# Performance work log

Hardware: AMD Instinct MI355X
Metric: run time of the kernel (lower is better)

Reference implementation:

```python
import jax, jax.numpy as jnp
import numpy as np

BATCH_SIZE = 4
TEMPERATURE = 0.07
NEG_MASK_VAL = -10.0


def setup_inputs() -> dict:
    key = jax.random.key(0)
    k1, k2 = jax.random.split(key)
    N, D = 16384, 256  # N = batch_size * n_patches
    feat_q = jax.random.normal(k1, (N, D), dtype=jnp.float32)
    feat_k = jax.random.normal(k2, (N, D), dtype=jnp.float32)
    return {"feat_q": feat_q, "feat_k": feat_k}


def reference(feat_q, feat_k):
    N, d = feat_q.shape
    feat_k = jax.lax.stop_gradient(feat_k)  # detach
    # positive logits: dot of matching rows -> [N, 1]
    l_pos = jnp.einsum('nd,nd->n', feat_q, feat_k)[:, None]
    q = feat_q.reshape(BATCH_SIZE, -1, d)  # [B, P, D]
    k = feat_k.reshape(BATCH_SIZE, -1, d)
    P = q.shape[1]
    # intra-batch-element negatives: [B, P, P]
    l_neg = jnp.einsum('bpd,bqd->bpq', q, k)
    eye = jnp.eye(P, dtype=bool)[None, :, :]
    l_neg = jnp.where(eye, jnp.float32(NEG_MASK_VAL), l_neg).reshape(-1, P)
    out = jnp.concatenate([l_pos, l_neg], axis=1) / TEMPERATURE  # [N, 1+P]
    # cross-entropy with target class 0, reduction='none'
    loss = -jax.nn.log_softmax(out, axis=1)[:, 0]
    return loss
```

## Files before the change

kernel.cpp:

```cpp
#include <hip/hip_runtime.h>
#include <hip/hip_bf16.h>


typedef __attribute__((ext_vector_type(8))) short short8;
typedef __attribute__((ext_vector_type(4))) float f32x4;

#define BATCH 4
#define PN 4096
#define DD 256
#define BN 64

constexpr float kLog2e = 1.4426950408889634f;
constexpr float kScale = kLog2e / 0.07f;
constexpr float kMask2 = -10.0f * kScale;
constexpr float kLn2   = 0.6931471805599453f;
constexpr float kNegInf = -3.0e38f;

__device__ __forceinline__ unsigned short f2bf(float f) {
  __hip_bfloat16 h = __float2bfloat16(f);
  return *reinterpret_cast<unsigned short*>(&h);
}
__device__ __forceinline__ float fexp2(float x) { return exp2f(x); }
__device__ __forceinline__ float flog2(float x) { return log2f(x); }

__global__ void k_convert(const float* __restrict__ src,
                          unsigned short* __restrict__ dst, int n4) {
  int i = blockIdx.x * blockDim.x + threadIdx.x;
  if (i >= n4) return;
  float4 v = reinterpret_cast<const float4*>(src)[i];
  ushort4 o;
  o.x = f2bf(v.x); o.y = f2bf(v.y); o.z = f2bf(v.z); o.w = f2bf(v.w);
  reinterpret_cast<ushort4*>(dst)[i] = o;
}

__device__ __forceinline__ void stage_tile(const char* __restrict__ src,
                                           char* ldsbase, int tid) {
  const int wv = tid >> 6;
#pragma unroll
  for (int ip = 0; ip < 8; ip++) {
    const int o   = ip * 4096 + tid * 16;
    const int row = o >> 9;
    const int so  = o ^ ((row & 15) << 4);
    __builtin_amdgcn_global_load_lds(
        (const __attribute__((address_space(1))) void*)(src + so),
        (__attribute__((address_space(3))) void*)(ldsbase + ip * 4096 + wv * 1024),
        16, 0, 0);
  }
}

__global__ __launch_bounds__(256, 2) void k_nce_split(
    const float* __restrict__ fq, const unsigned short* __restrict__ kb,
    float* __restrict__ pl, float* __restrict__ pp) {
  __shared__ __align__(16) char kt[2][BN * DD * 2];

  const int blk = blockIdx.x;
  const int b   = blk & 3;
  const int rt  = (blk >> 2) & 31;
  const int kc  = blk >> 7;
  const int R0  = rt * 128;
  const int tid = threadIdx.x;
  const int w   = tid >> 6;
  const int l   = tid & 63;
  const int g   = l >> 4;
  const int li  = l & 15;

  short8 a[2][8];
#pragma unroll
  for (int af = 0; af < 2; af++) {
    const float* qrow =
        fq + ((size_t)(b * PN + R0 + w * 32 + af * 16 + li)) * DD;
#pragma unroll
    for (int ks = 0; ks < 8; ks++) {
      const float* p = qrow + ks * 32 + g * 8;
      float4 v0 = *reinterpret_cast<const float4*>(p);
      float4 v1 = *reinterpret_cast<const float4*>(p + 4);
      a[af][ks][0] = (short)f2bf(v0.x * kScale);
      a[af][ks][1] = (short)f2bf(v0.y * kScale);
      a[af][ks][2] = (short)f2bf(v0.z * kScale);
      a[af][ks][3] = (short)f2bf(v0.w * kScale);
      a[af][ks][4] = (short)f2bf(v1.x * kScale);
      a[af][ks][5] = (short)f2bf(v1.y * kScale);
      a[af][ks][6] = (short)f2bf(v1.z * kScale);
      a[af][ks][7] = (short)f2bf(v1.w * kScale);
    }
  }

  float m[2][4], lsum[2][4], pos[2][4];
#pragma unroll
  for (int af = 0; af < 2; af++)
#pragma unroll
    for (int r = 0; r < 4; r++) {
      m[af][r] = kNegInf; lsum[af][r] = 0.f; pos[af][r] = kNegInf;
    }

  const char* ksrc = reinterpret_cast<const char*>(kb) +
                     (size_t)b * PN * 512 + (size_t)kc * 16 * 32768;
  const int diag_gt = (R0 + w * 32) >> 6;

  stage_tile(ksrc, kt[0], tid);
  __syncthreads();

  for (int ct = 0; ct < 16; ct++) {
    const int cur = ct & 1;
    if (ct + 1 < 16) stage_tile(ksrc + (size_t)(ct + 1) * 32768, kt[cur ^ 1], tid);

    const char* lb = kt[cur];
    f32x4 acc[2][4];
#pragma unroll
    for (int af = 0; af < 2; af++)
#pragma unroll
      for (int cf = 0; cf < 4; cf++) acc[af][cf] = f32x4{0.f, 0.f, 0.f, 0.f};

#pragma unroll
    for (int ks = 0; ks < 8; ks++) {
#pragma unroll
      for (int cf = 0; cf < 4; cf++) {
        const int row = cf * 16 + li;
        const int off = row * 512 + ((ks * 64 + g * 16) ^ ((row & 15) << 4));
        short8 bf = *reinterpret_cast<const short8*>(lb + off);
        acc[0][cf] =
            __builtin_amdgcn_mfma_f32_16x16x32_bf16(a[0][ks], bf, acc[0][cf], 0, 0, 0);
        acc[1][cf] =
            __builtin_amdgcn_mfma_f32_16x16x32_bf16(a[1][ks], bf, acc[1][cf], 0, 0, 0);
      }
    }

    const int gt = kc * 16 + ct;
    if (gt == diag_gt) {
#pragma unroll
      for (int af = 0; af < 2; af++) {
        const int cfd = ((w & 1) << 1) + af;
#pragma unroll
        for (int cf = 0; cf < 4; cf++)
          if (cf == cfd) {
#pragma unroll
            for (int r = 0; r < 4; r++)
              if (li == g * 4 + r) { pos[af][r] = acc[af][cf][r]; acc[af][cf][r] = kMask2; }
          }
      }
    }

#pragma unroll
    for (int af = 0; af < 2; af++)
#pragma unroll
      for (int r = 0; r < 4; r++) {
        float v0 = acc[af][0][r], v1 = acc[af][1][r];
        float v2 = acc[af][2][r], v3 = acc[af][3][r];
        float t0 = fmaxf(fmaxf(v0, v1), fmaxf(v2, v3));
        float mo = m[af][r];
        float mn = fmaxf(mo, t0);
        float s = fexp2(v0 - mn) + fexp2(v1 - mn) + fexp2(v2 - mn) + fexp2(v3 - mn);
        lsum[af][r] = lsum[af][r] * fexp2(mo - mn) + s;
        m[af][r] = mn;
      }
    __syncthreads();
  }

  const bool diag_chunk = (kc == (rt >> 3));
#pragma unroll
  for (int af = 0; af < 2; af++)
#pragma unroll
    for (int r = 0; r < 4; r++) {
      float m_ = m[af][r], l_ = lsum[af][r], p_ = pos[af][r];
#pragma unroll
      for (int off = 1; off < 16; off <<= 1) {
        float mo = __shfl_xor(m_, off, 64);
        float lo = __shfl_xor(l_, off, 64);
        float po = __shfl_xor(p_, off, 64);
        float mn = fmaxf(m_, mo);
        l_ = l_ * fexp2(m_ - mn) + lo * fexp2(mo - mn);
        m_ = mn;
        p_ = fmaxf(p_, po);
      }
      if (li == 0) {
        const int rowg = b * PN + R0 + w * 32 + af * 16 + g * 4 + r;
        pl[kc * (BATCH * PN) + rowg] = m_ + flog2(l_);
        if (diag_chunk) pp[rowg] = p_;
      }
    }
}

__global__ void k_combine(const float* __restrict__ pl,
                          const float* __restrict__ pp,
                          float* __restrict__ out) {
  const int i = blockIdx.x * blockDim.x + threadIdx.x;
  if (i >= BATCH * PN) return;
  float a0 = pl[i], a1 = pl[BATCH * PN + i];
  float a2 = pl[2 * BATCH * PN + i], a3 = pl[3 * BATCH * PN + i];
  float p = pp[i];
  float mm = fmaxf(fmaxf(a0, a1), fmaxf(a2, a3));
  float s = fexp2(a0 - mm) + fexp2(a1 - mm) + fexp2(a2 - mm) + fexp2(a3 - mm);
  float lse = mm + flog2(s);
  float mn = fmaxf(lse, p);
  float la = mn + flog2(fexp2(lse - mn) + fexp2(p - mn));
  out[i] = (la - p) * kLn2;
}

__global__ __launch_bounds__(256) void k_nce_full(const float* __restrict__ fq,
                                                  const unsigned short* __restrict__ kb,
                                                  float* __restrict__ out) {
  __shared__ __align__(16) char kt[2][BN * DD * 2];
  const int blk = blockIdx.x;
  const int b = blk & 3, rt = blk >> 2;
  const int R0 = rt * 64;
  const int tid = threadIdx.x;
  const int w = tid >> 6, l = tid & 63, g = l >> 4, li = l & 15;

  const float* qrow = fq + ((size_t)(b * PN + R0 + w * 16 + li)) * DD;
  short8 a[8];
#pragma unroll
  for (int ks = 0; ks < 8; ks++) {
    const float* p = qrow + ks * 32 + g * 8;
    float4 v0 = *reinterpret_cast<const float4*>(p);
    float4 v1 = *reinterpret_cast<const float4*>(p + 4);
    a[ks][0] = (short)f2bf(v0.x * kScale); a[ks][1] = (short)f2bf(v0.y * kScale);
    a[ks][2] = (short)f2bf(v0.z * kScale); a[ks][3] = (short)f2bf(v0.w * kScale);
    a[ks][4] = (short)f2bf(v1.x * kScale); a[ks][5] = (short)f2bf(v1.y * kScale);
    a[ks][6] = (short)f2bf(v1.z * kScale); a[ks][7] = (short)f2bf(v1.w * kScale);
  }
  float m[4], lsum[4], pos[4];
#pragma unroll
  for (int r = 0; r < 4; r++) { m[r] = kNegInf; lsum[r] = 0.f; pos[r] = kNegInf; }
  const char* ksrc = reinterpret_cast<const char*>(kb + (size_t)b * PN * DD);
  stage_tile(ksrc, kt[0], tid);
  __syncthreads();
  for (int ct = 0; ct < 64; ct++) {
    const int cur = ct & 1;
    if (ct + 1 < 64) stage_tile(ksrc + (size_t)(ct + 1) * 32768, kt[cur ^ 1], tid);
    const char* lb = kt[cur];
    f32x4 acc[4];
#pragma unroll
    for (int cf = 0; cf < 4; cf++) acc[cf] = f32x4{0.f, 0.f, 0.f, 0.f};
#pragma unroll
    for (int ks = 0; ks < 8; ks++) {
#pragma unroll
      for (int cf = 0; cf < 4; cf++) {
        const int row = cf * 16 + li;
        const int off = row * 512 + ((ks * 64 + g * 16) ^ ((row & 15) << 4));
        short8 bf = *reinterpret_cast<const short8*>(lb + off);
        acc[cf] = __builtin_amdgcn_mfma_f32_16x16x32_bf16(a[ks], bf, acc[cf], 0, 0, 0);
      }
    }
    if (ct == rt) {
#pragma unroll
      for (int cf = 0; cf < 4; cf++)
        if (cf == w) {
#pragma unroll
          for (int r = 0; r < 4; r++)
            if (li == g * 4 + r) { pos[r] = acc[cf][r]; acc[cf][r] = kMask2; }
        }
    }
#pragma unroll
    for (int r = 0; r < 4; r++) {
      float t0 = fmaxf(fmaxf(acc[0][r], acc[1][r]), fmaxf(acc[2][r], acc[3][r]));
      float mo = m[r];
      float mn = fmaxf(mo, t0);
      float s = fexp2(acc[0][r] - mn) + fexp2(acc[1][r] - mn) +
                fexp2(acc[2][r] - mn) + fexp2(acc[3][r] - mn);
      lsum[r] = lsum[r] * fexp2(mo - mn) + s;
      m[r] = mn;
    }
    __syncthreads();
  }
#pragma unroll
  for (int r = 0; r < 4; r++) {
    float m_ = m[r], l_ = lsum[r], p_ = pos[r];
#pragma unroll
    for (int off = 1; off < 16; off <<= 1) {
      float mo = __shfl_xor(m_, off, 64);
      float lo = __shfl_xor(l_, off, 64);
      float po = __shfl_xor(p_, off, 64);
      float mn = fmaxf(m_, mo);
      l_ = l_ * fexp2(m_ - mn) + lo * fexp2(mo - mn);
      m_ = mn;
      p_ = fmaxf(p_, po);
    }
    float mn  = fmaxf(m_, p_);
    float lse = mn + flog2(l_ * fexp2(m_ - mn) + fexp2(p_ - mn));
    if (li == 0) out[b * PN + R0 + w * 16 + g * 4 + r] = (lse - p_) * kLn2;
  }
}

extern "C" void kernel_launch(void* const* d_in, const int* in_sizes, int n_in,
                              void* d_out, int out_size, void* d_ws, size_t ws_size,
                              hipStream_t stream) {
  const float* fq = (const float*)d_in[0];
  const float* fk = (const float*)d_in[1];
  float* out = (float*)d_out;
  unsigned short* kb = (unsigned short*)d_ws;
  const size_t kbBytes = (size_t)BATCH * PN * DD * 2;
  const size_t plBytes = (size_t)4 * BATCH * PN * 4;
  const size_t ppBytes = (size_t)BATCH * PN * 4;

  const int n4 = (BATCH * PN * DD) / 4;
  hipLaunchKernelGGL(k_convert, dim3(n4 / 256), dim3(256), 0, stream, fk, kb, n4);

  if (ws_size >= kbBytes + plBytes + ppBytes) {
    float* pl = (float*)((char*)d_ws + kbBytes);
    float* pp = (float*)((char*)d_ws + kbBytes + plBytes);
    hipLaunchKernelGGL(k_nce_split, dim3(512), dim3(256), 0, stream, fq, kb, pl, pp);
    hipLaunchKernelGGL(k_combine, dim3((BATCH * PN) / 256), dim3(256), 0, stream,
                       pl, pp, out);
  } else {
    hipLaunchKernelGGL(k_nce_full, dim3(BATCH * (PN / 64)), dim3(256), 0, stream,
                       fq, kb, out);
  }
}
```

Before: 67.67 us.

## Enlarge row tile to 256 with 8-way column split to improve LDS reuse

Adds a new kernel in which each block processes 256 query rows (64 per wave, four A fragments) against a 512-column chunk of keys, giving an 8-way column split. Each B fragment read from LDS now feeds four MFMAs instead of two, which halves LDS traffic per FLOP and halves total key-tile staging. The first key tile load is also issued before the query conversion so the two overlap. In exchange, register pressure rises (4x8 A fragments plus 16 accumulators) and the combine kernel must merge 8 partial log-sum-exps instead of 4.

```diff
diff --git a/kernel.cpp b/kernel.cpp
--- a/kernel.cpp
+++ b/kernel.cpp
@@ -9,6 +9,7 @@
 #define PN 4096
 #define DD 256
 #define BN 64
+#define NP (BATCH * PN)
 
 constexpr float kLog2e = 1.4426950408889634f;
 constexpr float kScale = kLog2e / 0.07f;
@@ -48,27 +49,34 @@
   }
 }
 
-__global__ __launch_bounds__(256, 2) void k_nce_split(
+__global__ __launch_bounds__(256, 2) void k_nce4(
     const float* __restrict__ fq, const unsigned short* __restrict__ kb,
     float* __restrict__ pl, float* __restrict__ pp) {
   __shared__ __align__(16) char kt[2][BN * DD * 2];
 
   const int blk = blockIdx.x;
   const int b   = blk & 3;
-  const int rt  = (blk >> 2) & 31;
-  const int kc  = blk >> 7;
-  const int R0  = rt * 128;
+  const int r2  = blk >> 2;
+  const int rt  = r2 & 15;
+  const int kc  = r2 >> 4;
+  const int R0  = rt * 256;
+  const int C0  = kc * 512;
   const int tid = threadIdx.x;
   const int w   = tid >> 6;
   const int l   = tid & 63;
   const int g   = l >> 4;
   const int li  = l & 15;
 
-  short8 a[2][8];
-#pragma unroll
-  for (int af = 0; af < 2; af++) {
+  const char* ksrc = reinterpret_cast<const char*>(kb) +
+                     ((size_t)b * PN + C0) * 512;
+
+  stage_tile(ksrc, kt[0], tid);
+
+  short8 a[4][8];
+#pragma unroll
+  for (int af = 0; af < 4; af++) {
     const float* qrow =
-        fq + ((size_t)(b * PN + R0 + w * 32 + af * 16 + li)) * DD;
+        fq + ((size_t)(b * PN + R0 + w * 64 + af * 16 + li)) * DD;
 #pragma unroll
     for (int ks = 0; ks < 8; ks++) {
       const float* p = qrow + ks * 32 + g * 8;
@@ -85,29 +93,26 @@
     }
   }
 
-  float m[2][4], lsum[2][4], pos[2][4];
-#pragma unroll
-  for (int af = 0; af < 2; af++)
+  float m[4][4], lsum[4][4], pos[4][4];
+#pragma unroll
+  for (int af = 0; af < 4; af++)
 #pragma unroll
     for (int r = 0; r < 4; r++) {
       m[af][r] = kNegInf; lsum[af][r] = 0.f; pos[af][r] = kNegInf;
     }
 
-  const char* ksrc = reinterpret_cast<const char*>(kb) +
-                     (size_t)b * PN * 512 + (size_t)kc * 16 * 32768;
-  const int diag_gt = (R0 + w * 32) >> 6;
-
-  stage_tile(ksrc, kt[0], tid);
+  const int ctd = (kc == (rt >> 1)) ? ((rt & 1) * 4 + w) : -1;
+
   __syncthreads();
 
-  for (int ct = 0; ct < 16; ct++) {
+  for (int ct = 0; ct < 8; ct++) {
     const int cur = ct & 1;
-    if (ct + 1 < 16) stage_tile(ksrc + (size_t)(ct + 1) * 32768, kt[cur ^ 1], tid);
+    if (ct + 1 < 8) stage_tile(ksrc + (size_t)(ct + 1) * 32768, kt[cur ^ 1], tid);
 
     const char* lb = kt[cur];
-    f32x4 acc[2][4];
-#pragma unroll
-    for (int af = 0; af < 2; af++)
+    f32x4 acc[4][4];
+#pragma unroll
+    for (int af = 0; af < 4; af++)
 #pragma unroll
       for (int cf = 0; cf < 4; cf++) acc[af][cf] = f32x4{0.f, 0.f, 0.f, 0.f};
 
@@ -118,30 +123,23 @@
         const int row = cf * 16 + li;
         const int off = row * 512 + ((ks * 64 + g * 16) ^ ((row & 15) << 4));
         short8 bf = *reinterpret_cast<const short8*>(lb + off);
-        acc[0][cf] =
-            __builtin_amdgcn_mfma_f32_16x16x32_bf16(a[0][ks], bf, acc[0][cf], 0, 0, 0);
-        acc[1][cf] =
-            __builtin_amdgcn_mfma_f32_16x16x32_bf16(a[1][ks], bf, acc[1][cf], 0, 0, 0);
-      }
-    }
-
-    const int gt = kc * 16 + ct;
-    if (gt == diag_gt) {
-#pragma unroll
-      for (int af = 0; af < 2; af++) {
-        const int cfd = ((w & 1) << 1) + af;
-#pragma unroll
-        for (int cf = 0; cf < 4; cf++)
-          if (cf == cfd) {
-#pragma unroll
-            for (int r = 0; r < 4; r++)
-              if (li == g * 4 + r) { pos[af][r] = acc[af][cf][r]; acc[af][cf][r] = kMask2; }
-          }
-      }
-    }
-
-#pragma unroll
-    for (int af = 0; af < 2; af++)
+#pragma unroll
+        for (int af = 0; af < 4; af++)
+          acc[af][cf] = __builtin_amdgcn_mfma_f32_16x16x32_bf16(a[af][ks], bf,
+                                                               acc[af][cf], 0, 0, 0);
+      }
+    }
+
+    if (ct == ctd) {
+#pragma unroll
+      for (int af = 0; af < 4; af++)
+#pragma unroll
+        for (int r = 0; r < 4; r++)
+          if (li == g * 4 + r) { pos[af][r] = acc[af][af][r]; acc[af][af][r] = kMask2; }
+    }
+
+#pragma unroll
+    for (int af = 0; af < 4; af++)
 #pragma unroll
       for (int r = 0; r < 4; r++) {
         float v0 = acc[af][0][r], v1 = acc[af][1][r];
@@ -156,9 +154,9 @@
     __syncthreads();
   }
 
-  const bool diag_chunk = (kc == (rt >> 3));
-#pragma unroll
-  for (int af = 0; af < 2; af++)
+  const bool diag_chunk = (kc == (rt >> 1));
+#pragma unroll
+  for (int af = 0; af < 4; af++)
 #pragma unroll
     for (int r = 0; r < 4; r++) {
       float m_ = m[af][r], l_ = lsum[af][r], p_ = pos[af][r];
@@ -173,27 +171,145 @@
         p_ = fmaxf(p_, po);
       }
       if (li == 0) {
-        const int rowg = b * PN + R0 + w * 32 + af * 16 + g * 4 + r;
-        pl[kc * (BATCH * PN) + rowg] = m_ + flog2(l_);
+        const int rowg = b * PN + R0 + w * 64 + af * 16 + g * 4 + r;
+        pl[kc * NP + rowg] = m_ + flog2(l_);
         if (diag_chunk) pp[rowg] = p_;
       }
     }
 }
 
+template <int NC>
 __global__ void k_combine(const float* __restrict__ pl,
                           const float* __restrict__ pp,
                           float* __restrict__ out) {
   const int i = blockIdx.x * blockDim.x + threadIdx.x;
-  if (i >= BATCH * PN) return;
-  float a0 = pl[i], a1 = pl[BATCH * PN + i];
-  float a2 = pl[2 * BATCH * PN + i], a3 = pl[3 * BATCH * PN + i];
+  if (i >= NP) return;
+  float mm = kNegInf;
+  float v[NC];
+#pragma unroll
+  for (int c = 0; c < NC; c++) { v[c] = pl[c * NP + i]; mm = fmaxf(mm, v[c]); }
+  float s = 0.f;
+#pragma unroll
+  for (int c = 0; c < NC; c++) s += fexp2(v[c] - mm);
+  float lse = mm + flog2(s);
   float p = pp[i];
-  float mm = fmaxf(fmaxf(a0, a1), fmaxf(a2, a3));
-  float s = fexp2(a0 - mm) + fexp2(a1 - mm) + fexp2(a2 - mm) + fexp2(a3 - mm);
-  float lse = mm + flog2(s);
   float mn = fmaxf(lse, p);
   float la = mn + flog2(fexp2(lse - mn) + fexp2(p - mn));
   out[i] = (la - p) * kLn2;
+}
+
+__global__ __launch_bounds__(256, 2) void k_nce_split(
+    const float* __restrict__ fq, const unsigned short* __restrict__ kb,
+    float* __restrict__ pl, float* __restrict__ pp) {
+  __shared__ __align__(16) char kt[2][BN * DD * 2];
+  const int blk = blockIdx.x;
+  const int b   = blk & 3;
+  const int rt  = (blk >> 2) & 31;
+  const int kc  = blk >> 7;
+  const int R0  = rt * 128;
+  const int tid = threadIdx.x;
+  const int w   = tid >> 6;
+  const int l   = tid & 63;
+  const int g   = l >> 4;
+  const int li  = l & 15;
+
+  short8 a[2][8];
+#pragma unroll
+  for (int af = 0; af < 2; af++) {
+    const float* qrow = fq + ((size_t)(b * PN + R0 + w * 32 + af * 16 + li)) * DD;
+#pragma unroll
+    for (int ks = 0; ks < 8; ks++) {
+      const float* p = qrow + ks * 32 + g * 8;
+      float4 v0 = *reinterpret_cast<const float4*>(p);
+      float4 v1 = *reinterpret_cast<const float4*>(p + 4);
+      a[af][ks][0] = (short)f2bf(v0.x * kScale); a[af][ks][1] = (short)f2bf(v0.y * kScale);
+      a[af][ks][2] = (short)f2bf(v0.z * kScale); a[af][ks][3] = (short)f2bf(v0.w * kScale);
+      a[af][ks][4] = (short)f2bf(v1.x * kScale); a[af][ks][5] = (short)f2bf(v1.y * kScale);
+      a[af][ks][6] = (short)f2bf(v1.z * kScale); a[af][ks][7] = (short)f2bf(v1.w * kScale);
+    }
+  }
+  float m[2][4], lsum[2][4], pos[2][4];
+#pragma unroll
+  for (int af = 0; af < 2; af++)
+#pragma unroll
+    for (int r = 0; r < 4; r++) { m[af][r] = kNegInf; lsum[af][r] = 0.f; pos[af][r] = kNegInf; }
+
+  const char* ksrc = reinterpret_cast<const char*>(kb) +
+                     (size_t)b * PN * 512 + (size_t)kc * 16 * 32768;
+  const int diag_gt = (R0 + w * 32) >> 6;
+  stage_tile(ksrc, kt[0], tid);
+  __syncthreads();
+  for (int ct = 0; ct < 16; ct++) {
+    const int cur = ct & 1;
+    if (ct + 1 < 16) stage_tile(ksrc + (size_t)(ct + 1) * 32768, kt[cur ^ 1], tid);
+    const char* lb = kt[cur];
+    f32x4 acc[2][4];
+#pragma unroll
+    for (int af = 0; af < 2; af++)
+#pragma unroll
+      for (int cf = 0; cf < 4; cf++) acc[af][cf] = f32x4{0.f, 0.f, 0.f, 0.f};
+#pragma unroll
+    for (int ks = 0; ks < 8; ks++) {
+#pragma unroll
+      for (int cf = 0; cf < 4; cf++) {
+        const int row = cf * 16 + li;
+        const int off = row * 512 + ((ks * 64 + g * 16) ^ ((row & 15) << 4));
+        short8 bf = *reinterpret_cast<const short8*>(lb + off);
+        acc[0][cf] = __builtin_amdgcn_mfma_f32_16x16x32_bf16(a[0][ks], bf, acc[0][cf], 0, 0, 0);
+        acc[1][cf] = __builtin_amdgcn_mfma_f32_16x16x32_bf16(a[1][ks], bf, acc[1][cf], 0, 0, 0);
+      }
+    }
+    const int gt = kc * 16 + ct;
+    if (gt == diag_gt) {
+#pragma unroll
+      for (int af = 0; af < 2; af++) {
+        const int cfd = ((w & 1) << 1) + af;
+#pragma unroll
+        for (int cf = 0; cf < 4; cf++)
+          if (cf == cfd) {
+#pragma unroll
+            for (int r = 0; r < 4; r++)
+              if (li == g * 4 + r) { pos[af][r] = acc[af][cf][r]; acc[af][cf][r] = kMask2; }
+          }
+      }
+    }
+#pragma unroll
+    for (int af = 0; af < 2; af++)
+#pragma unroll
+      for (int r = 0; r < 4; r++) {
+        float v0 = acc[af][0][r], v1 = acc[af][1][r];
+        float v2 = acc[af][2][r], v3 = acc[af][3][r];
+        float t0 = fmaxf(fmaxf(v0, v1), fmaxf(v2, v3));
+        float mo = m[af][r];
+        float mn = fmaxf(mo, t0);
+        float s = fexp2(v0 - mn) + fexp2(v1 - mn) + fexp2(v2 - mn) + fexp2(v3 - mn);
+        lsum[af][r] = lsum[af][r] * fexp2(mo - mn) + s;
+        m[af][r] = mn;
+      }
+    __syncthreads();
+  }
+  const bool diag_chunk = (kc == (rt >> 3));
+#pragma unroll
+  for (int af = 0; af < 2; af++)
+#pragma unroll
+    for (int r = 0; r < 4; r++) {
+      float m_ = m[af][r], l_ = lsum[af][r], p_ = pos[af][r];
+#pragma unroll
+      for (int off = 1; off < 16; off <<= 1) {
+        float mo = __shfl_xor(m_, off, 64);
+        float lo = __shfl_xor(l_, off, 64);
+        float po = __shfl_xor(p_, off, 64);
+        float mn = fmaxf(m_, mo);
+        l_ = l_ * fexp2(m_ - mn) + lo * fexp2(mo - mn);
+        m_ = mn;
+        p_ = fmaxf(p_, po);
+      }
+      if (li == 0) {
+        const int rowg = b * PN + R0 + w * 32 + af * 16 + g * 4 + r;
+        pl[kc * NP + rowg] = m_ + flog2(l_);
+        if (diag_chunk) pp[rowg] = p_;
+      }
+    }
 }
 
 __global__ __launch_bounds__(256) void k_nce_full(const float* __restrict__ fq,
@@ -288,19 +404,24 @@
   const float* fk = (const float*)d_in[1];
   float* out = (float*)d_out;
   unsigned short* kb = (unsigned short*)d_ws;
-  const size_t kbBytes = (size_t)BATCH * PN * DD * 2;
-  const size_t plBytes = (size_t)4 * BATCH * PN * 4;
-  const size_t ppBytes = (size_t)BATCH * PN * 4;
-
-  const int n4 = (BATCH * PN * DD) / 4;
+  const size_t kbBytes = (size_t)NP * DD * 2;
+  const size_t ppBytes = (size_t)NP * 4;
+  const size_t pl8Bytes = (size_t)8 * NP * 4;
+  const size_t pl4Bytes = (size_t)4 * NP * 4;
+
+  const int n4 = (NP * DD) / 4;
   hipLaunchKernelGGL(k_convert, dim3(n4 / 256), dim3(256), 0, stream, fk, kb, n4);
 
-  if (ws_size >= kbBytes + plBytes + ppBytes) {
+  if (ws_size >= kbBytes + pl8Bytes + ppBytes) {
     float* pl = (float*)((char*)d_ws + kbBytes);
-    float* pp = (float*)((char*)d_ws + kbBytes + plBytes);
+    float* pp = (float*)((char*)d_ws + kbBytes + pl8Bytes);
+    hipLaunchKernelGGL(k_nce4, dim3(512), dim3(256), 0, stream, fq, kb, pl, pp);
+    hipLaunchKernelGGL(k_combine<8>, dim3(NP / 256), dim3(256), 0, stream, pl, pp, out);
+  } else if (ws_size >= kbBytes + pl4Bytes + ppBytes) {
+    float* pl = (float*)((char*)d_ws + kbBytes);
+    float* pp = (float*)((char*)d_ws + kbBytes + pl4Bytes);
     hipLaunchKernelGGL(k_nce_split, dim3(512), dim3(256), 0, stream, fq, kb, pl, pp);
-    hipLaunchKernelGGL(k_combine, dim3((BATCH * PN) / 256), dim3(256), 0, stream,
-                       pl, pp, out);
+    hipLaunchKernelGGL(k_combine<4>, dim3(NP / 256), dim3(256), 0, stream, pl, pp, out);
   } else {
     hipLaunchKernelGGL(k_nce_full, dim3(BATCH * (PN / 64)), dim3(256), 0, stream,
                        fq, kb, out);
```

After: 100.4 us. +48.4%, slower.
